# Kernel optimization log

Measured on AMD Instinct MI355X. Metric: run time of the kernel, lower is better.

The kernel has to match this reference:

```python
import jax, jax.numpy as jnp
import numpy as np

N_HEAD, D_MODEL, D_HEAD = 16, 1024, 64
BSZ, SEQLEN = 2, 2048
ROPE_BASE = 10000.0


def _rope_tables(seqlen, d_head, base=ROPE_BASE):
    # freqs_cis = exp(i * t * theta_j), theta_j = base^(-2j/d_head)
    inv_freq = 1.0 / (base ** (np.arange(0, d_head, 2, dtype=np.float32) / d_head))
    t = np.arange(seqlen, dtype=np.float32)
    ang = np.outer(t, inv_freq)  # [S, d_head//2]
    return jnp.asarray(np.cos(ang)), jnp.asarray(np.sin(ang))


def setup_inputs() -> dict:
    key = jax.random.key(0)
    ks = jax.random.split(key, 5)
    x = jax.random.normal(ks[0], (BSZ, SEQLEN, D_MODEL), dtype=jnp.float32)
    freqs_cos, freqs_sin = _rope_tables(SEQLEN, D_HEAD)
    scale = 0.02
    # weights stored as (in, out) so projection is x @ w
    wq = jax.random.normal(ks[1], (D_MODEL, N_HEAD * D_HEAD), dtype=jnp.float32) * scale
    wk = jax.random.normal(ks[2], (D_MODEL, N_HEAD * D_HEAD), dtype=jnp.float32) * scale
    wv = jax.random.normal(ks[3], (D_MODEL, N_HEAD * D_HEAD), dtype=jnp.float32) * scale
    wo = jax.random.normal(ks[4], (N_HEAD * D_HEAD, D_MODEL), dtype=jnp.float32) * scale
    return {"x": x, "freqs_cos": freqs_cos, "freqs_sin": freqs_sin,
            "wq": wq, "wk": wk, "wv": wv, "wo": wo}


def _apply_rope(t, cos, sin):
    # t: [B, S, H, Dh]; complex pairs are consecutive elements (x0 + i*x1)
    B, S, H, Dh = t.shape
    tf = t.astype(jnp.float32).reshape(B, S, H, Dh // 2, 2)
    t0, t1 = tf[..., 0], tf[..., 1]
    c = cos[None, :, None, :]  # [1, S, 1, Dh//2]
    s = sin[None, :, None, :]
    o0 = t0 * c - t1 * s
    o1 = t0 * s + t1 * c
    return jnp.stack([o0, o1], axis=-1).reshape(B, S, H, Dh).astype(t.dtype)


def reference(x, freqs_cos, freqs_sin, wq, wk, wv, wo):
    B, S, _ = x.shape
    H, Dh = N_HEAD, D_HEAD
    q = jnp.einsum('bsd,de->bse', x, wq).reshape(B, S, H, Dh)
    k = jnp.einsum('bsd,de->bse', x, wk).reshape(B, S, H, Dh)
    v = jnp.einsum('bsd,de->bse', x, wv).reshape(B, S, H, Dh)
    q = _apply_rope(q, freqs_cos, freqs_sin)
    k = _apply_rope(k, freqs_cos, freqs_sin)
    # [B, H, S, Dh]
    q = q.transpose(0, 2, 1, 3)
    k = k.transpose(0, 2, 1, 3)
    v = v.transpose(0, 2, 1, 3)
    scores = jnp.einsum('bhqd,bhkd->bhqk', q, k) / jnp.sqrt(jnp.float32(Dh))
    probs = jax.nn.softmax(scores.astype(jnp.float32), axis=-1).astype(q.dtype)
    out = jnp.einsum('bhqk,bhkd->bhqd', probs, v)  # [B, H, S, Dh]
    out = out.transpose(0, 2, 1, 3).reshape(B, S, H * Dh)
    return jnp.einsum('bse,ed->bsd', out, wo)
```

## Files before the change

kernel.cpp:

```cpp
#include <hip/hip_runtime.h>
#include <math.h>

#define BSZ 2
#define SEQ 2048
#define NH 16
#define DH 64
#define DM 1024
#define HD 1024

typedef _Float16 h16;
typedef _Float16 half8 __attribute__((ext_vector_type(8)));
typedef _Float16 half4 __attribute__((ext_vector_type(4)));
typedef float f32x4 __attribute__((ext_vector_type(4)));

__device__ __forceinline__ f32x4 mfma16(half8 a, half8 b, f32x4 c) {
    return __builtin_amdgcn_mfma_f32_16x16x32_f16(a, b, c, 0, 0, 0);
}

__device__ __forceinline__ void async_copy16(h16* lds, const h16* g) {
    __builtin_amdgcn_global_load_lds(
        (const __attribute__((address_space(1))) unsigned int*)g,
        (__attribute__((address_space(3))) unsigned int*)lds, 16, 0, 0);
}

#define SWZ(cb, r) ((((cb) ^ ((r) & 7)) * 8))

__global__ __launch_bounds__(256) void prep_kernel(
    const float* __restrict__ x, const float* __restrict__ wq,
    const float* __restrict__ wk, const float* __restrict__ wv,
    const float* __restrict__ wo,
    h16* __restrict__ x16, h16* __restrict__ wt)
{
    const int z = blockIdx.z;
    const int t = threadIdx.x;
    if (z == 4) {
        int flat = blockIdx.y * 16 + blockIdx.x;
#pragma unroll
        for (int i = 0; i < 8; ++i) {
            int idx = flat * 16384 + i * 2048 + t * 8;
            float4 a = *(const float4*)&x[idx];
            float4 b = *(const float4*)&x[idx + 4];
            half8 o;
            o[0] = (h16)a.x; o[1] = (h16)a.y; o[2] = (h16)a.z; o[3] = (h16)a.w;
            o[4] = (h16)b.x; o[5] = (h16)b.y; o[6] = (h16)b.z; o[7] = (h16)b.w;
            *(half8*)&x16[idx] = o;
        }
        return;
    }
    const float* w = (z == 0) ? wq : (z == 1) ? wk : (z == 2) ? wv : wo;
    h16* ot = wt + (size_t)z * DM * DM;
    __shared__ float tile[64][68];
    const int k0 = blockIdx.y * 64, n0 = blockIdx.x * 64;
    const int r = t >> 2, c4 = (t & 3) * 16;
#pragma unroll
    for (int i = 0; i < 16; i += 4) {
        float4 v = *(const float4*)&w[(size_t)(k0 + r) * DM + n0 + c4 + i];
        tile[r][c4 + i + 0] = v.x; tile[r][c4 + i + 1] = v.y;
        tile[r][c4 + i + 2] = v.z; tile[r][c4 + i + 3] = v.w;
    }
    __syncthreads();
#pragma unroll
    for (int g = 0; g < 2; ++g) {
        half8 hh;
#pragma unroll
        for (int j = 0; j < 8; ++j)
            hh[j] = (h16)tile[c4 + g * 8 + j][r];
        *(half8*)&ot[(size_t)(n0 + r) * DM + k0 + c4 + g * 8] = hh;
    }
}

__global__ __launch_bounds__(512, 4) void qkv_kernel(
    const h16* __restrict__ x16, const h16* __restrict__ wt,
    const float* __restrict__ fcos, const float* __restrict__ fsin,
    h16* __restrict__ Q16, h16* __restrict__ K16, h16* __restrict__ VT16)
{
    const int z = blockIdx.z;
    const h16* __restrict__ bw = wt + (size_t)z * DM * DM;

    __shared__ h16 smem[17408];
    h16* As = smem;
    h16* Bs = smem + 8192;
    h16* Vt = smem;

    const int m0 = blockIdx.y * 128;
    const int n0 = blockIdx.x * 128;
    const int t  = threadIdx.x;
    const int w  = t >> 6, ln = t & 63;
    const int L  = ln & 15, U = ln >> 4;
    const int wm = (w & 3) * 32;
    const int wn = (w >> 2) * 64;

    const int sr  = ln >> 3;
    const int scb = (ln & 7) ^ sr;

    f32x4 acc[2][4];
#pragma unroll
    for (int i = 0; i < 2; ++i)
#pragma unroll
        for (int j = 0; j < 4; ++j) acc[i][j] = (f32x4)0.0f;

    for (int k0 = 0; k0 < DM; k0 += 64) {
        __syncthreads();
#pragma unroll
        for (int c = 0; c < 2; ++c) {
            int rb = w * 16 + c * 8;
            async_copy16(&As[rb * 64], &x16[(size_t)(m0 + rb + sr) * DM + k0 + scb * 8]);
            async_copy16(&Bs[rb * 64], &bw [(size_t)(n0 + rb + sr) * DM + k0 + scb * 8]);
        }
        __syncthreads();

#pragma unroll
        for (int ks = 0; ks < 2; ++ks) {
            half8 af[2], bf[4];
#pragma unroll
            for (int mt = 0; mt < 2; ++mt)
                af[mt] = *(const half8*)&As[(wm + mt * 16 + L) * 64 + SWZ(ks * 4 + U, L)];
#pragma unroll
            for (int nt = 0; nt < 4; ++nt)
                bf[nt] = *(const half8*)&Bs[(wn + nt * 16 + L) * 64 + SWZ(ks * 4 + U, L)];
#pragma unroll
            for (int mt = 0; mt < 2; ++mt)
#pragma unroll
                for (int nt = 0; nt < 4; ++nt)
                    acc[mt][nt] = mfma16(bf[nt], af[mt], acc[mt][nt]);
        }
    }

    const int b = m0 >> 11;
    const int sbase = m0 & 2047;

    if (z < 2) {
        const float sc = (z == 0) ? 0.125f * 1.44269504088896f : 1.0f;
#pragma unroll
        for (int mt = 0; mt < 2; ++mt) {
            int s = sbase + wm + mt * 16 + L;
            const float* ct = &fcos[s * 32];
            const float* st = &fsin[s * 32];
#pragma unroll
            for (int nt = 0; nt < 4; ++nt) {
                int nl = n0 + wn + nt * 16 + U * 4;
                int d = nl & 63, h = nl >> 6;
                int pd = d >> 1;
                float cv0 = ct[pd], sv0 = st[pd];
                float cv1 = ct[pd + 1], sv1 = st[pd + 1];
                float v0 = acc[mt][nt][0], v1 = acc[mt][nt][1];
                float v2 = acc[mt][nt][2], v3 = acc[mt][nt][3];
                float o0 = (v0 * cv0 - v1 * sv0) * sc;
                float o1 = (v0 * sv0 + v1 * cv0) * sc;
                float o2 = (v2 * cv1 - v3 * sv1) * sc;
                float o3 = (v2 * sv1 + v3 * cv1) * sc;
                size_t addr = ((size_t)(b * NH + h) * SEQ + s) * DH + d;
                half4 kk;
                kk[0] = (h16)o0; kk[1] = (h16)o1; kk[2] = (h16)o2; kk[3] = (h16)o3;
                if (z == 0) *(half4*)&Q16[addr] = kk;
                else        *(half4*)&K16[addr] = kk;
            }
        }
    } else {
        __syncthreads();
#pragma unroll
        for (int mt = 0; mt < 2; ++mt)
#pragma unroll
            for (int nt = 0; nt < 4; ++nt)
#pragma unroll
                for (int r = 0; r < 4; ++r) {
                    int nloc = wn + nt * 16 + U * 4 + r;
                    int sloc = wm + mt * 16 + L;
                    Vt[nloc * 136 + sloc] = (h16)acc[mt][nt][r];
                }
        __syncthreads();
#pragma unroll
        for (int i = 0; i < 4; ++i) {
            int c = i * 512 + t;
            int dl = c >> 4;
            int s8 = (c & 15) * 8;
            half8 vv = *(const half8*)&Vt[dl * 136 + s8];
            int n = n0 + dl;
            int d = n & 63, h = n >> 6;
            *(half8*)&VT16[((size_t)(b * NH + h) * DH + d) * SEQ + sbase + s8] = vv;
        }
    }
}

#define PLD 136

__global__ __launch_bounds__(512, 4) void attn_kernel(
    const h16* __restrict__ Q16, const h16* __restrict__ K16,
    const h16* __restrict__ VT16, h16* __restrict__ A16)
{
    __shared__ h16 Ks[128 * 64];
    __shared__ h16 VTs[64 * 128];
    __shared__ __align__(16) h16 Ps[128 * PLD];
    __shared__ float lbuf[8][2][16];

    float* Obuf = (float*)Ps;

    const int t = threadIdx.x, w = t >> 6, ln = t & 63;
    const int L = ln & 15, U = ln >> 4;
    const int pair = w >> 1, half = w & 1;
    const int qw = pair * 32, kh = half * 64;
    const int q0 = blockIdx.x * 128;
    const int bh = blockIdx.y;
    const size_t base = (size_t)bh * SEQ * DH;

    half8 qf[2][2];
#pragma unroll
    for (int qb = 0; qb < 2; ++qb)
#pragma unroll
        for (int ks = 0; ks < 2; ++ks)
            qf[qb][ks] = *(const half8*)&Q16[base + (size_t)(q0 + qw + qb * 16 + L) * DH + ks * 32 + U * 8];

    half8 one8;
#pragma unroll
    for (int i = 0; i < 8; ++i) one8[i] = (h16)1.0f;

    f32x4 O[4][2];
    f32x4 lsum[2];
#pragma unroll
    for (int dt = 0; dt < 4; ++dt)
#pragma unroll
        for (int qb = 0; qb < 2; ++qb) O[dt][qb] = (f32x4)0.0f;
    lsum[0] = (f32x4)0.0f;
    lsum[1] = (f32x4)0.0f;

    const int sr  = ln >> 3;
    const int scb = (ln & 7) ^ sr;

    for (int j0 = 0; j0 < SEQ; j0 += 128) {
        __syncthreads();
#pragma unroll
        for (int c = 0; c < 2; ++c) {
            int rbk = c * 64 + w * 8;
            async_copy16(&Ks[rbk * 64], &K16[base + (size_t)(j0 + rbk + sr) * DH + scb * 8]);
        }
#pragma unroll
        for (int c = 0; c < 2; ++c) {
            int rv = (w * 2 + c) * 4;
            int c16 = (ln & 15) ^ ((rv + U) & 15);
            async_copy16(&VTs[rv * 128], &VT16[base + (size_t)(rv + U) * SEQ + j0 + c16 * 8]);
        }
        __syncthreads();

        f32x4 S[4][2];
#pragma unroll
        for (int nt = 0; nt < 4; ++nt) {
            S[nt][0] = (f32x4)0.0f;
            S[nt][1] = (f32x4)0.0f;
#pragma unroll
            for (int ks = 0; ks < 2; ++ks) {
                half8 kf = *(const half8*)&Ks[(kh + nt * 16 + L) * 64 + SWZ(ks * 4 + U, L)];
                S[nt][0] = mfma16(kf, qf[0][ks], S[nt][0]);
                S[nt][1] = mfma16(kf, qf[1][ks], S[nt][1]);
            }
        }

#pragma unroll
        for (int qb = 0; qb < 2; ++qb) {
            int prow = (qw + qb * 16 + L) * PLD + kh;
#pragma unroll
            for (int nt = 0; nt < 4; ++nt) {
                half4 pq;
                pq[0] = (h16)exp2f(S[nt][qb][0]);
                pq[1] = (h16)exp2f(S[nt][qb][1]);
                pq[2] = (h16)exp2f(S[nt][qb][2]);
                pq[3] = (h16)exp2f(S[nt][qb][3]);
                *(half4*)&Ps[prow + nt * 16 + U * 4] = pq;
            }
        }

        half8 pf[2][2];
#pragma unroll
        for (int qb = 0; qb < 2; ++qb)
#pragma unroll
            for (int ks2 = 0; ks2 < 2; ++ks2)
                pf[qb][ks2] = *(const half8*)&Ps[(qw + qb * 16 + L) * PLD + kh + ks2 * 32 + U * 8];
#pragma unroll
        for (int dt = 0; dt < 4; ++dt)
#pragma unroll
            for (int ks2 = 0; ks2 < 2; ++ks2) {
                half8 vf = *(const half8*)&VTs[(dt * 16 + L) * 128 + ((half * 8 + ks2 * 4 + U) ^ L) * 8];
                O[dt][0] = mfma16(vf, pf[0][ks2], O[dt][0]);
                O[dt][1] = mfma16(vf, pf[1][ks2], O[dt][1]);
            }
#pragma unroll
        for (int ks2 = 0; ks2 < 2; ++ks2) {
            lsum[0] = mfma16(one8, pf[0][ks2], lsum[0]);
            lsum[1] = mfma16(one8, pf[1][ks2], lsum[1]);
        }
    }

    if (U == 0) {
        lbuf[w][0][L] = lsum[0][0];
        lbuf[w][1][L] = lsum[1][0];
    }
    __syncthreads();
    const int pw = w ^ 1;
    float l_tot[2];
#pragma unroll
    for (int qb = 0; qb < 2; ++qb)
        l_tot[qb] = lsum[qb][0] + lbuf[pw][qb][L];

    if (half) {
#pragma unroll
        for (int qb = 0; qb < 2; ++qb)
#pragma unroll
            for (int dt = 0; dt < 4; ++dt)
                *(f32x4*)&Obuf[(qw + qb * 16 + L) * 68 + dt * 16 + U * 4] = O[dt][qb];
    }
    __syncthreads();
    if (!half) {
        const int b = bh >> 4, hh = bh & 15;
#pragma unroll
        for (int qb = 0; qb < 2; ++qb) {
            float inv = 1.0f / l_tot[qb];
            int s = q0 + qw + qb * 16 + L;
#pragma unroll
            for (int dt = 0; dt < 4; ++dt) {
                f32x4 op = *(const f32x4*)&Obuf[(qw + qb * 16 + L) * 68 + dt * 16 + U * 4];
                half4 o4;
#pragma unroll
                for (int r = 0; r < 4; ++r)
                    o4[r] = (h16)((O[dt][qb][r] + op[r]) * inv);
                *(half4*)&A16[(size_t)(b * SEQ + s) * HD + hh * DH + dt * 16 + U * 4] = o4;
            }
        }
    }
}

__global__ __launch_bounds__(512, 4) void oproj_kernel(
    const h16* __restrict__ A16, const h16* __restrict__ bw,
    float* __restrict__ out)
{
    __shared__ h16 As[128 * 64];
    __shared__ h16 Bs[64 * 64];

    const int m0 = blockIdx.y * 128;
    const int n0 = blockIdx.x * 64;
    const int t  = threadIdx.x;
    const int w  = t >> 6, ln = t & 63;
    const int L  = ln & 15, U = ln >> 4;

    const int sr  = ln >> 3;
    const int scb = (ln & 7) ^ sr;

    f32x4 acc[4];
#pragma unroll
    for (int j = 0; j < 4; ++j) acc[j] = (f32x4)0.0f;

    for (int k0 = 0; k0 < DM; k0 += 64) {
        __syncthreads();
#pragma unroll
        for (int c = 0; c < 2; ++c) {
            int rb = w * 16 + c * 8;
            async_copy16(&As[rb * 64], &A16[(size_t)(m0 + rb + sr) * DM + k0 + scb * 8]);
        }
        {
            int rb = w * 8;
            async_copy16(&Bs[rb * 64], &bw[(size_t)(n0 + rb + sr) * DM + k0 + scb * 8]);
        }
        __syncthreads();

#pragma unroll
        for (int ks = 0; ks < 2; ++ks) {
            half8 af, bf[4];
            af = *(const half8*)&As[(w * 16 + L) * 64 + SWZ(ks * 4 + U, L)];
#pragma unroll
            for (int nt = 0; nt < 4; ++nt)
                bf[nt] = *(const half8*)&Bs[(nt * 16 + L) * 64 + SWZ(ks * 4 + U, L)];
#pragma unroll
            for (int nt = 0; nt < 4; ++nt)
                acc[nt] = mfma16(af, bf[nt], acc[nt]);
        }
    }

#pragma unroll
    for (int nt = 0; nt < 4; ++nt)
#pragma unroll
        for (int r = 0; r < 4; ++r) {
            int row = m0 + w * 16 + U * 4 + r;
            int col = n0 + nt * 16 + L;
            out[(size_t)row * DM + col] = acc[nt][r];
        }
}

extern "C" void kernel_launch(void* const* d_in, const int* in_sizes, int n_in,
                              void* d_out, int out_size, void* d_ws, size_t ws_size,
                              hipStream_t stream)
{
    const float* x    = (const float*)d_in[0];
    const float* fcos = (const float*)d_in[1];
    const float* fsin = (const float*)d_in[2];
    const float* wq   = (const float*)d_in[3];
    const float* wk   = (const float*)d_in[4];
    const float* wv   = (const float*)d_in[5];
    const float* wo   = (const float*)d_in[6];
    float* out = (float*)d_out;

    const size_t M4 = (size_t)4 * 1024 * 1024;
    h16* x16  = (h16*)d_ws;
    h16* wt   = x16 + M4;
    h16* Q16  = wt + M4;
    h16* K16  = Q16 + M4;
    h16* VT16 = K16 + M4;
    h16* A16  = VT16 + M4;

    prep_kernel<<<dim3(16, 16, 5), 256, 0, stream>>>(x, wq, wk, wv, wo, x16, wt);
    qkv_kernel<<<dim3(8, 32, 3), 512, 0, stream>>>(x16, wt, fcos, fsin,
                                                   Q16, K16, VT16);
    attn_kernel<<<dim3(16, 32), 512, 0, stream>>>(Q16, K16, VT16, A16);
    oproj_kernel<<<dim3(16, 32), 512, 0, stream>>>(A16, wt + 3 * (size_t)DM * DM, out);
}
```

Baseline: 208.9 us.

## Double-buffer V tiles and prefetch K/V in attention loop with swizzled P

Restructures the attention main loop so the next V^T tile is prefetched into a second LDS buffer and the next K tile is loaded right after QK^T finishes, overlapping global loads with compute instead of doing two full barriers per iteration. The P buffer and output scratch switch from padded rows to XOR-swizzled layouts to avoid bank conflicts while fitting the extra V buffer in a single shared array. It also uses the raw hardware exp2 intrinsic and raises wave priority around the MFMA sections. The risks are higher LDS use, which may lower occupancy, and more delicate hand-placed waitcnt and barrier ordering.

```diff
diff --git a/kernel.cpp b/kernel.cpp
--- a/kernel.cpp
+++ b/kernel.cpp
@@ -24,6 +24,11 @@
 }
 
 #define SWZ(cb, r) ((((cb) ^ ((r) & 7)) * 8))
+
+#define PSA(r, c) ((r) * 128 + (((((c) >> 3) ^ ((r) & 15)) << 3) | ((c) & 7)))
+#define OBA(r, c) ((r) * 64 + ((((c) >> 2) ^ ((r) & 15)) << 2))
+
+#define EXP2(x) __builtin_amdgcn_exp2f(x)
 
 __global__ __launch_bounds__(256) void prep_kernel(
     const float* __restrict__ x, const float* __restrict__ wq,
@@ -182,17 +187,15 @@
     }
 }
 
-#define PLD 136
-
 __global__ __launch_bounds__(512, 4) void attn_kernel(
     const h16* __restrict__ Q16, const h16* __restrict__ K16,
     const h16* __restrict__ VT16, h16* __restrict__ A16)
 {
-    __shared__ h16 Ks[128 * 64];
-    __shared__ h16 VTs[64 * 128];
-    __shared__ __align__(16) h16 Ps[128 * PLD];
-    __shared__ float lbuf[8][2][16];
-
+    __shared__ h16 smem[40960];
+    h16* Ks  = smem;
+    h16* VTs = smem + 8192;
+    h16* Ps  = smem + 24576;
+    float* lbuf = (float*)smem;
     float* Obuf = (float*)Ps;
 
     const int t = threadIdx.x, w = t >> 6, ln = t & 63;
@@ -226,22 +229,39 @@
     const int sr  = ln >> 3;
     const int scb = (ln & 7) ^ sr;
 
+#pragma unroll
+    for (int c = 0; c < 2; ++c) {
+        int rv = (w * 2 + c) * 4;
+        int c16 = (ln & 15) ^ ((rv + U) & 15);
+        async_copy16(&VTs[rv * 128], &VT16[base + (size_t)(rv + U) * SEQ + c16 * 8]);
+    }
+#pragma unroll
+    for (int c = 0; c < 2; ++c) {
+        int rbk = c * 64 + w * 8;
+        async_copy16(&Ks[rbk * 64], &K16[base + (size_t)(rbk + sr) * DH + scb * 8]);
+    }
+
     for (int j0 = 0; j0 < SEQ; j0 += 128) {
-        __syncthreads();
-#pragma unroll
-        for (int c = 0; c < 2; ++c) {
-            int rbk = c * 64 + w * 8;
-            async_copy16(&Ks[rbk * 64], &K16[base + (size_t)(j0 + rbk + sr) * DH + scb * 8]);
-        }
-#pragma unroll
-        for (int c = 0; c < 2; ++c) {
-            int rv = (w * 2 + c) * 4;
-            int c16 = (ln & 15) ^ ((rv + U) & 15);
-            async_copy16(&VTs[rv * 128], &VT16[base + (size_t)(rv + U) * SEQ + j0 + c16 * 8]);
-        }
-        __syncthreads();
+        const int buf = (j0 >> 7) & 1;
+        h16* VTcur = VTs + buf * 8192;
+
+        asm volatile("s_waitcnt vmcnt(0)" ::: "memory");
+        __builtin_amdgcn_s_barrier();
+        __builtin_amdgcn_sched_barrier(0);
+
+        if (j0 + 128 < SEQ) {
+            h16* VTnxt = VTs + (buf ^ 1) * 8192;
+#pragma unroll
+            for (int c = 0; c < 2; ++c) {
+                int rv = (w * 2 + c) * 4;
+                int c16 = (ln & 15) ^ ((rv + U) & 15);
+                async_copy16(&VTnxt[rv * 128],
+                             &VT16[base + (size_t)(rv + U) * SEQ + (j0 + 128) + c16 * 8]);
+            }
+        }
 
         f32x4 S[4][2];
+        __builtin_amdgcn_s_setprio(1);
 #pragma unroll
         for (int nt = 0; nt < 4; ++nt) {
             S[nt][0] = (f32x4)0.0f;
@@ -253,18 +273,32 @@
                 S[nt][1] = mfma16(kf, qf[1][ks], S[nt][1]);
             }
         }
+        __builtin_amdgcn_s_setprio(0);
+
+        asm volatile("s_waitcnt lgkmcnt(0)" ::: "memory");
+        __builtin_amdgcn_sched_barrier(0);
+        __builtin_amdgcn_s_barrier();
+
+        if (j0 + 128 < SEQ) {
+#pragma unroll
+            for (int c = 0; c < 2; ++c) {
+                int rbk = c * 64 + w * 8;
+                async_copy16(&Ks[rbk * 64],
+                             &K16[base + (size_t)(j0 + 128 + rbk + sr) * DH + scb * 8]);
+            }
+        }
 
 #pragma unroll
         for (int qb = 0; qb < 2; ++qb) {
-            int prow = (qw + qb * 16 + L) * PLD + kh;
+            int prow = qw + qb * 16 + L;
 #pragma unroll
             for (int nt = 0; nt < 4; ++nt) {
                 half4 pq;
-                pq[0] = (h16)exp2f(S[nt][qb][0]);
-                pq[1] = (h16)exp2f(S[nt][qb][1]);
-                pq[2] = (h16)exp2f(S[nt][qb][2]);
-                pq[3] = (h16)exp2f(S[nt][qb][3]);
-                *(half4*)&Ps[prow + nt * 16 + U * 4] = pq;
+                pq[0] = (h16)EXP2(S[nt][qb][0]);
+                pq[1] = (h16)EXP2(S[nt][qb][1]);
+                pq[2] = (h16)EXP2(S[nt][qb][2]);
+                pq[3] = (h16)EXP2(S[nt][qb][3]);
+                *(half4*)&Ps[PSA(prow, kh + nt * 16 + U * 4)] = pq;
             }
         }
 
@@ -273,12 +307,14 @@
         for (int qb = 0; qb < 2; ++qb)
 #pragma unroll
             for (int ks2 = 0; ks2 < 2; ++ks2)
-                pf[qb][ks2] = *(const half8*)&Ps[(qw + qb * 16 + L) * PLD + kh + ks2 * 32 + U * 8];
+                pf[qb][ks2] = *(const half8*)&Ps[PSA(qw + qb * 16 + L, kh + ks2 * 32 + U * 8)];
+
+        __builtin_amdgcn_s_setprio(1);
 #pragma unroll
         for (int dt = 0; dt < 4; ++dt)
 #pragma unroll
             for (int ks2 = 0; ks2 < 2; ++ks2) {
-                half8 vf = *(const half8*)&VTs[(dt * 16 + L) * 128 + ((half * 8 + ks2 * 4 + U) ^ L) * 8];
+                half8 vf = *(const half8*)&VTcur[(dt * 16 + L) * 128 + ((half * 8 + ks2 * 4 + U) ^ L) * 8];
                 O[dt][0] = mfma16(vf, pf[0][ks2], O[dt][0]);
                 O[dt][1] = mfma16(vf, pf[1][ks2], O[dt][1]);
             }
@@ -287,25 +323,25 @@
             lsum[0] = mfma16(one8, pf[0][ks2], lsum[0]);
             lsum[1] = mfma16(one8, pf[1][ks2], lsum[1]);
         }
+        __builtin_amdgcn_s_setprio(0);
     }
 
     if (U == 0) {
-        lbuf[w][0][L] = lsum[0][0];
-        lbuf[w][1][L] = lsum[1][0];
+        lbuf[w * 32 + L]      = lsum[0][0];
+        lbuf[w * 32 + 16 + L] = lsum[1][0];
     }
     __syncthreads();
     const int pw = w ^ 1;
     float l_tot[2];
-#pragma unroll
-    for (int qb = 0; qb < 2; ++qb)
-        l_tot[qb] = lsum[qb][0] + lbuf[pw][qb][L];
+    l_tot[0] = lsum[0][0] + lbuf[pw * 32 + L];
+    l_tot[1] = lsum[1][0] + lbuf[pw * 32 + 16 + L];
 
     if (half) {
 #pragma unroll
         for (int qb = 0; qb < 2; ++qb)
 #pragma unroll
             for (int dt = 0; dt < 4; ++dt)
-                *(f32x4*)&Obuf[(qw + qb * 16 + L) * 68 + dt * 16 + U * 4] = O[dt][qb];
+                *(f32x4*)&Obuf[OBA(qw + qb * 16 + L, dt * 16 + U * 4)] = O[dt][qb];
     }
     __syncthreads();
     if (!half) {
@@ -316,7 +352,7 @@
             int s = q0 + qw + qb * 16 + L;
 #pragma unroll
             for (int dt = 0; dt < 4; ++dt) {
-                f32x4 op = *(const f32x4*)&Obuf[(qw + qb * 16 + L) * 68 + dt * 16 + U * 4];
+                f32x4 op = *(const f32x4*)&Obuf[OBA(qw + qb * 16 + L, dt * 16 + U * 4)];
                 half4 o4;
 #pragma unroll
                 for (int r = 0; r < 4; ++r)
```

New measurement: 187.5 us. -10.2%, faster.
